# Kernel tuning notes

Hardware: AMD Instinct MI355X
Metric: run time of the kernel (lower is better)

## Reference

```python
import jax, jax.numpy as jnp
import numpy as np
from math import sqrt

D_MODEL = 1024
B, T = 4, 4096


def setup_inputs() -> dict:
    key = jax.random.key(0)
    kx, kqk, kvo = jax.random.split(key, 3)
    x = jax.random.normal(kx, (B, T, D_MODEL), dtype=jnp.float32)
    # xavier_uniform for square [D, D]: limit = sqrt(6 / (D + D))
    limit = sqrt(6.0 / (2 * D_MODEL))
    QK = jax.random.uniform(kqk, (D_MODEL, D_MODEL), minval=-limit, maxval=limit, dtype=jnp.float32)
    VO = jax.random.uniform(kvo, (D_MODEL, D_MODEL), minval=-limit, maxval=limit, dtype=jnp.float32)
    return {"x": x, "QK": QK, "VO": VO}


def reference(x, QK, VO):
    d_model = QK.shape[0]
    # scores[b,t,u] = x[b,t,:] @ QK @ x[b,u,:]  -- precompute xQK once
    xQK = jnp.einsum('btd,de->bte', x, QK)                 # [B,T,D]
    scores = jnp.einsum('bte,bue->btu', xQK, x) / sqrt(d_model)  # [B,T,T]
    attn = jax.nn.softmax(scores, axis=2)
    # out[b,t,e] = attn @ x @ VO
    av = jnp.einsum('btu,bud->btd', attn, x)               # [B,T,D]
    return jnp.einsum('btd,de->bte', av, VO)
```

## Files before the change

### kernel.cpp

```cpp
#include <hip/hip_runtime.h>
#include <hip/hip_bf16.h>


#define BB 4
#define TT 4096
#define DD 1024

typedef __attribute__((ext_vector_type(8))) short bf16x8;
typedef __attribute__((ext_vector_type(4))) float f32x4;

__device__ __forceinline__ void gll16(const void* g, void* l) {
  __builtin_amdgcn_global_load_lds(
      (__attribute__((address_space(1))) void*)g,
      (__attribute__((address_space(3))) void*)l, 16, 0, 0);
}

#define WAIT_VM(n) asm volatile("s_waitcnt vmcnt(" #n ")" ::: "memory")
#define WAIT_LGKM0 do { asm volatile("s_waitcnt lgkmcnt(0)" ::: "memory"); \
                        __builtin_amdgcn_sched_barrier(0); } while (0)
#define BARRIER    __builtin_amdgcn_s_barrier()

__global__ __launch_bounds__(256) void xprep_k(const float* __restrict__ in,
                                               __hip_bfloat16* __restrict__ rm,
                                               __hip_bfloat16* __restrict__ cm,
                                               int R, int C, long bs) {
  in += (long)blockIdx.z * bs; rm += (long)blockIdx.z * bs; cm += (long)blockIdx.z * bs;
  __shared__ __hip_bfloat16 tile[64][65];
  int c0 = blockIdx.x * 64, r0 = blockIdx.y * 64;
  int tx = threadIdx.x & 63, ty = threadIdx.x >> 6;
#pragma unroll
  for (int i = 0; i < 16; ++i) {
    int r = ty + i * 4;
    __hip_bfloat16 v = __float2bfloat16(in[(long)(r0 + r) * C + c0 + tx]);
    tile[r][tx] = v;
    rm[(long)(r0 + r) * C + c0 + tx] = v;
  }
  __syncthreads();
#pragma unroll
  for (int i = 0; i < 16; ++i) {
    int c = ty + i * 4;
    cm[(long)(c0 + c) * R + r0 + tx] = tile[tx][c];
  }
}

__global__ __launch_bounds__(256) void transpose_cast_k(const float* __restrict__ in,
                                                        __hip_bfloat16* __restrict__ out,
                                                        int R, int C) {
  __shared__ __hip_bfloat16 tile[64][65];
  int c0 = blockIdx.x * 64, r0 = blockIdx.y * 64;
  int tx = threadIdx.x & 63, ty = threadIdx.x >> 6;
#pragma unroll
  for (int i = 0; i < 16; ++i) {
    int r = ty + i * 4;
    tile[r][tx] = __float2bfloat16(in[(long)(r0 + r) * C + c0 + tx]);
  }
  __syncthreads();
#pragma unroll
  for (int i = 0; i < 16; ++i) {
    int c = ty + i * 4;
    out[(long)(c0 + c) * R + r0 + tx] = tile[tx][c];
  }
}

__global__ __launch_bounds__(256) void zero_f32_k(float* __restrict__ p, int n) {
  int i = blockIdx.x * 256 + threadIdx.x;
  if (i < n) p[i] = 0.f;
}

template <typename OUT_T, int EPI>
__global__ __launch_bounds__(512, 2) void gemm256(
    const __hip_bfloat16* __restrict__ A,
    const __hip_bfloat16* __restrict__ Bt,
    OUT_T* __restrict__ C,
    int M, int N, int K, float alpha,
    long sAz, long sBz, long sCz, float* __restrict__ lsum,
    int cx, int cy) {
  __shared__ alignas(16) char smem[131072];
  A  += (long)blockIdx.z * sAz;
  Bt += (long)blockIdx.z * sBz;
  C  += (long)blockIdx.z * sCz;

  const int lin = blockIdx.x + gridDim.x * blockIdx.y;
  const int xcd = lin & 7;
  const int s   = lin >> 3;
  const int rpc = cx * cy;
  const int r   = xcd + 8 * (s / rpc);
  const int p   = s % rpc;
  const int rx  = gridDim.x / cx;
  const int bx  = (r % rx) * cx + p % cx;
  const int by  = (r / rx) * cy + p / cx;

  const int tid  = threadIdx.x;
  const int lane = tid & 63;
  const int wid  = tid >> 6;
  const int wr   = wid >> 2;
  const int wc   = wid & 3;
  const long m0 = (long)bx * 256;
  const long n0 = (long)by * 256;
  const int NT = K >> 6;

  const int srow = tid >> 3;
  const int sswz = (tid & 7) ^ (srow & 7);
  const __hip_bfloat16* gA = A  + (m0 + srow) * (long)K + sswz * 8;
  const __hip_bfloat16* gB = Bt + (n0 + srow) * (long)K + sswz * 8;

#define STG_A(s_, c_, D_) gll16(gA + (long)(c_) * 64 * K + (long)(s_) * 64, \
                                smem + (D_) + (c_) * 8192 + wid * 1024)
#define STG_B(s_, c_, D_) gll16(gB + (long)(c_) * 64 * K + (long)(s_) * 64, \
                                smem + (D_) + 32768 + (c_) * 8192 + wid * 1024)

  const int fr = lane & 15, l4 = lane >> 4, f7 = lane & 7;
  const char* a00 = smem +         (wr * 128 + fr) * 128 + ((l4    ) ^ f7) * 16;
  const char* a01 = smem +         (wr * 128 + fr) * 128 + ((4 | l4) ^ f7) * 16;
  const char* b00 = smem + 32768 + (wc * 64  + fr) * 128 + ((l4    ) ^ f7) * 16;
  const char* b01 = smem + 32768 + (wc * 64  + fr) * 128 + ((4 | l4) ^ f7) * 16;
  const char* a10 = a00 + 65536; const char* a11 = a01 + 65536;
  const char* b10 = b00 + 65536; const char* b11 = b01 + 65536;

  bf16x8 aq[4][2], bq[4][2];
#define RD_A(p0, p1, MIOFF)                                         \
  _Pragma("unroll") for (int mi_ = 0; mi_ < 4; ++mi_) {             \
    aq[mi_][0] = *(const bf16x8*)((p0) + ((MIOFF) + mi_) * 2048);   \
    aq[mi_][1] = *(const bf16x8*)((p1) + ((MIOFF) + mi_) * 2048);   \
  }
#define RD_B(p0, p1, NI0)                                           \
  _Pragma("unroll") for (int ni_ = 0; ni_ < 2; ++ni_) {             \
    bq[(NI0) + ni_][0] = *(const bf16x8*)((p0) + ((NI0) + ni_) * 2048); \
    bq[(NI0) + ni_][1] = *(const bf16x8*)((p1) + ((NI0) + ni_) * 2048); \
  }

  f32x4 acc[8][4];
#pragma unroll
  for (int mi = 0; mi < 8; ++mi)
#pragma unroll
    for (int ni = 0; ni < 4; ++ni)
      acc[mi][ni] = (f32x4){0.f, 0.f, 0.f, 0.f};

#define MFMA16(MI0, NI0)                                                       \
  do {                                                                         \
    __builtin_amdgcn_s_setprio(1);                                             \
    _Pragma("unroll") for (int ks_ = 0; ks_ < 2; ++ks_)                        \
    _Pragma("unroll") for (int mi_ = 0; mi_ < 4; ++mi_)                        \
    _Pragma("unroll") for (int ni_ = 0; ni_ < 2; ++ni_)                        \
      acc[(MI0) + mi_][(NI0) + ni_] = __builtin_amdgcn_mfma_f32_16x16x32_bf16( \
          aq[mi_][ks_], bq[(NI0) + ni_][ks_], acc[(MI0) + mi_][(NI0) + ni_],   \
          0, 0, 0);                                                            \
    __builtin_amdgcn_s_setprio(0);                                             \
  } while (0)

#pragma unroll
  for (int c = 0; c < 4; ++c) STG_A(0, c, 0);
#pragma unroll
  for (int c = 0; c < 4; ++c) STG_B(0, c, 0);
  STG_B(1, 0, 65536); STG_B(1, 1, 65536);
  WAIT_VM(2);
  BARRIER;

  for (int t2 = 0; t2 < NT; t2 += 2) {
    const bool g = (t2 + 2 < NT);
    RD_A(a00, a01, 0); RD_B(b00, b01, 0);
    STG_B(t2 + 1, 2, 65536); STG_B(t2 + 1, 3, 65536);
    STG_A(t2 + 1, 0, 65536); STG_A(t2 + 1, 1, 65536);
    asm volatile("s_waitcnt lgkmcnt(8)");
    BARRIER; WAIT_LGKM0; MFMA16(0, 0);
    RD_B(b00, b01, 2);
    STG_A(t2 + 1, 2, 65536); STG_A(t2 + 1, 3, 65536);
    BARRIER; WAIT_LGKM0; MFMA16(0, 2);
    RD_A(a00, a01, 4);
    BARRIER; WAIT_LGKM0; MFMA16(4, 2);
    if (g) { STG_B(t2 + 2, 0, 0); STG_B(t2 + 2, 1, 0); WAIT_VM(2); }
    else   { WAIT_VM(0); }
    BARRIER; MFMA16(4, 0);
    RD_A(a10, a11, 0); RD_B(b10, b11, 0);
    if (g) { STG_B(t2 + 2, 2, 0); STG_B(t2 + 2, 3, 0);
             STG_A(t2 + 2, 0, 0); STG_A(t2 + 2, 1, 0); }
    asm volatile("s_waitcnt lgkmcnt(8)");
    BARRIER; WAIT_LGKM0; MFMA16(0, 0);
    RD_B(b10, b11, 2);
    if (g) { STG_A(t2 + 2, 2, 0); STG_A(t2 + 2, 3, 0); }
    BARRIER; WAIT_LGKM0; MFMA16(0, 2);
    RD_A(a10, a11, 4);
    BARRIER; WAIT_LGKM0; MFMA16(4, 2);
    if (g) { STG_B(t2 + 3, 0, 65536); STG_B(t2 + 3, 1, 65536); WAIT_VM(2); }
    BARRIER; MFMA16(4, 0);
  }

  if constexpr (EPI == 2) {
    float* lred = (float*)smem;
    __syncthreads();
    for (int i = tid; i < 1024; i += 512) lred[i] = 0.f;
    __syncthreads();
#pragma unroll
    for (int mi = 0; mi < 8; ++mi) {
#pragma unroll
      for (int r_ = 0; r_ < 4; ++r_) {
        const int rloc = wr * 128 + mi * 16 + (l4 << 2) + r_;
        const long row = m0 + rloc;
        float rs = 0.f;
#pragma unroll
        for (int ni = 0; ni < 4; ++ni) {
          float e = __expf(acc[mi][ni][r_] * alpha);
          long col = n0 + wc * 64 + ni * 16 + fr;
          C[row * (long)N + col] = (OUT_T)__float2bfloat16(e);
          rs += e;
        }
        rs += __shfl_xor(rs, 1); rs += __shfl_xor(rs, 2);
        rs += __shfl_xor(rs, 4); rs += __shfl_xor(rs, 8);
        if (fr == 0) lred[rloc * 4 + wc] = rs;
      }
    }
    __syncthreads();
    if (tid < 256) {
      float s4 = lred[tid * 4] + lred[tid * 4 + 1] + lred[tid * 4 + 2] + lred[tid * 4 + 3];
      atomicAdd(&lsum[(long)blockIdx.z * M + m0 + tid], s4);
    }
  } else if constexpr (EPI == 3) {
#pragma unroll
    for (int mi = 0; mi < 8; ++mi) {
      const long row = m0 + wr * 128 + mi * 16 + (l4 << 2);
      float4 lv = *(const float4*)&lsum[(long)blockIdx.z * M + row];
      float inv[4] = {1.f / lv.x, 1.f / lv.y, 1.f / lv.z, 1.f / lv.w};
#pragma unroll
      for (int ni = 0; ni < 4; ++ni) {
        long col = n0 + wc * 64 + ni * 16 + fr;
#pragma unroll
        for (int r_ = 0; r_ < 4; ++r_)
          C[(row + r_) * (long)N + col] = (OUT_T)__float2bfloat16(acc[mi][ni][r_] * inv[r_]);
      }
    }
  } else {
#pragma unroll
    for (int mi = 0; mi < 8; ++mi)
#pragma unroll
      for (int ni = 0; ni < 4; ++ni)
#pragma unroll
        for (int r_ = 0; r_ < 4; ++r_) {
          long row = m0 + wr * 128 + mi * 16 + (l4 << 2) + r_;
          long col = n0 + wc * 64 + ni * 16 + fr;
          float v = acc[mi][ni][r_] * alpha;
          if constexpr (EPI == 0)
            C[row * (long)N + col] = v;
          else
            C[row * (long)N + col] = (OUT_T)__float2bfloat16(v);
        }
  }
#undef STG_A
#undef STG_B
#undef RD_A
#undef RD_B
#undef MFMA16
}

extern "C" void kernel_launch(void* const* d_in, const int* in_sizes, int n_in,
                              void* d_out, int out_size, void* d_ws, size_t ws_size,
                              hipStream_t stream) {
  const float* x  = (const float*)d_in[0];
  const float* QK = (const float*)d_in[1];
  const float* VO = (const float*)d_in[2];
  char* ws = (char*)d_ws;

  const long MB = 1l << 20;
  __hip_bfloat16* QKT  = (__hip_bfloat16*)(ws);
  float*          lsum = (float*)(ws);
  __hip_bfloat16* VOT  = (__hip_bfloat16*)(ws + 2 * MB);
  __hip_bfloat16* xb   = (__hip_bfloat16*)(ws + 4 * MB);
  __hip_bfloat16* xT   = (__hip_bfloat16*)(ws + 36 * MB);
  __hip_bfloat16* attn = (__hip_bfloat16*)(ws + 68 * MB);
  __hip_bfloat16* xqk  = (__hip_bfloat16*)d_out;

  const long NTOK = (long)BB * TT;
  const long bstride = (long)TT * DD;
  const long aslot = (long)TT * TT;

  xprep_k<<<dim3(DD / 64, TT / 64, BB), 256, 0, stream>>>(x, xb, xT, TT, DD, bstride);
  transpose_cast_k<<<dim3(16, 16, 1), 256, 0, stream>>>(QK, QKT, DD, DD);
  transpose_cast_k<<<dim3(16, 16, 1), 256, 0, stream>>>(VO, VOT, DD, DD);

  gemm256<__hip_bfloat16, 1><<<dim3(TT / 256, DD / 256, BB), 512, 0, stream>>>(
      xb, QKT, xqk, TT, DD, DD, 1.0f, bstride, 0, bstride, nullptr, 2, 4);

  zero_f32_k<<<(int)(NTOK / 256), 256, 0, stream>>>(lsum, (int)NTOK);

  gemm256<__hip_bfloat16, 2><<<dim3(TT / 256, TT / 256, BB), 512, 0, stream>>>(
      xqk, xb, attn, TT, TT, DD, 0.03125f, bstride, bstride, aslot, lsum, 4, 8);

  gemm256<__hip_bfloat16, 3><<<dim3(TT / 256, DD / 256, BB), 512, 0, stream>>>(
      attn, xT, xb, TT, DD, TT, 1.0f, aslot, bstride, bstride, lsum, 2, 4);

  gemm256<float, 0><<<dim3((int)(NTOK / 256), DD / 256, 1), 512, 0, stream>>>(
      xb, VOT, (float*)d_out, (int)NTOK, DD, DD, 1.0f, 0, 0, 0, nullptr, 8, 4);
}
```

Before: 336.1 us.

## Software-pipeline LDS fragment reads ahead of MFMA blocks with double-buffered registers

Restructures the GEMM main loop so LDS reads for the next MFMA sub-block are issued before the current MFMA sub-block runs. A full 8-row A fragment set and two ping-pong B fragment buffers replace the single-use register arrays. Global-to-LDS staging of the next tile is reordered and waits are retuned, with A of tile 1 now prefetched in the prologue. The goal is to hide LDS latency behind matrix math, at the cost of more VGPRs and a trickier ordering of barriers and waits.

```diff
diff --git a/kernel.cpp b/kernel.cpp
--- a/kernel.cpp
+++ b/kernel.cpp
@@ -19,6 +19,7 @@
 #define WAIT_LGKM0 do { asm volatile("s_waitcnt lgkmcnt(0)" ::: "memory"); \
                         __builtin_amdgcn_sched_barrier(0); } while (0)
 #define BARRIER    __builtin_amdgcn_s_barrier()
+#define SB0        __builtin_amdgcn_sched_barrier(0)
 
 __global__ __launch_bounds__(256) void xprep_k(const float* __restrict__ in,
                                                __hip_bfloat16* __restrict__ rm,
@@ -117,16 +118,19 @@
   const char* a10 = a00 + 65536; const char* a11 = a01 + 65536;
   const char* b10 = b00 + 65536; const char* b11 = b01 + 65536;
 
-  bf16x8 aq[4][2], bq[4][2];
-#define RD_A(p0, p1, MIOFF)                                         \
-  _Pragma("unroll") for (int mi_ = 0; mi_ < 4; ++mi_) {             \
-    aq[mi_][0] = *(const bf16x8*)((p0) + ((MIOFF) + mi_) * 2048);   \
-    aq[mi_][1] = *(const bf16x8*)((p1) + ((MIOFF) + mi_) * 2048);   \
-  }
-#define RD_B(p0, p1, NI0)                                           \
-  _Pragma("unroll") for (int ni_ = 0; ni_ < 2; ++ni_) {             \
-    bq[(NI0) + ni_][0] = *(const bf16x8*)((p0) + ((NI0) + ni_) * 2048); \
-    bq[(NI0) + ni_][1] = *(const bf16x8*)((p1) + ((NI0) + ni_) * 2048); \
+  bf16x8 aq[8][2];
+  bf16x8 bqA[2][2];
+  bf16x8 bqB[2][2];
+
+#define RD_A4(p0, p1, MI0)                                                 \
+  _Pragma("unroll") for (int mi_ = 0; mi_ < 4; ++mi_) {                    \
+    aq[(MI0) + mi_][0] = *(const bf16x8*)((p0) + ((MI0) + mi_) * 2048);    \
+    aq[(MI0) + mi_][1] = *(const bf16x8*)((p1) + ((MI0) + mi_) * 2048);    \
+  }
+#define RD_B2(p0, p1, BQ, NB)                                              \
+  _Pragma("unroll") for (int ni_ = 0; ni_ < 2; ++ni_) {                    \
+    BQ[ni_][0] = *(const bf16x8*)((p0) + ((NB) + ni_) * 2048);             \
+    BQ[ni_][1] = *(const bf16x8*)((p1) + ((NB) + ni_) * 2048);             \
   }
 
   f32x4 acc[8][4];
@@ -136,14 +140,14 @@
     for (int ni = 0; ni < 4; ++ni)
       acc[mi][ni] = (f32x4){0.f, 0.f, 0.f, 0.f};
 
-#define MFMA16(MI0, NI0)                                                       \
+#define MFMA16(MI0, NI0, BQ)                                                   \
   do {                                                                         \
     __builtin_amdgcn_s_setprio(1);                                             \
     _Pragma("unroll") for (int ks_ = 0; ks_ < 2; ++ks_)                        \
     _Pragma("unroll") for (int mi_ = 0; mi_ < 4; ++mi_)                        \
     _Pragma("unroll") for (int ni_ = 0; ni_ < 2; ++ni_)                        \
       acc[(MI0) + mi_][(NI0) + ni_] = __builtin_amdgcn_mfma_f32_16x16x32_bf16( \
-          aq[mi_][ks_], bq[(NI0) + ni_][ks_], acc[(MI0) + mi_][(NI0) + ni_],   \
+          aq[(MI0) + mi_][ks_], BQ[ni_][ks_], acc[(MI0) + mi_][(NI0) + ni_],   \
           0, 0, 0);                                                            \
     __builtin_amdgcn_s_setprio(0);                                             \
   } while (0)
@@ -152,37 +156,60 @@
   for (int c = 0; c < 4; ++c) STG_A(0, c, 0);
 #pragma unroll
   for (int c = 0; c < 4; ++c) STG_B(0, c, 0);
+  STG_A(1, 0, 65536); STG_A(1, 1, 65536);
+  STG_A(1, 2, 65536); STG_A(1, 3, 65536);
   STG_B(1, 0, 65536); STG_B(1, 1, 65536);
-  WAIT_VM(2);
+  WAIT_VM(6);
   BARRIER;
+  RD_A4(a00, a01, 0);
+  RD_B2(b00, b01, bqA, 0);
 
   for (int t2 = 0; t2 < NT; t2 += 2) {
     const bool g = (t2 + 2 < NT);
-    RD_A(a00, a01, 0); RD_B(b00, b01, 0);
+    BARRIER; WAIT_LGKM0;
+    RD_A4(a00, a01, 4);
     STG_B(t2 + 1, 2, 65536); STG_B(t2 + 1, 3, 65536);
-    STG_A(t2 + 1, 0, 65536); STG_A(t2 + 1, 1, 65536);
-    asm volatile("s_waitcnt lgkmcnt(8)");
-    BARRIER; WAIT_LGKM0; MFMA16(0, 0);
-    RD_B(b00, b01, 2);
-    STG_A(t2 + 1, 2, 65536); STG_A(t2 + 1, 3, 65536);
-    BARRIER; WAIT_LGKM0; MFMA16(0, 2);
-    RD_A(a00, a01, 4);
-    BARRIER; WAIT_LGKM0; MFMA16(4, 2);
-    if (g) { STG_B(t2 + 2, 0, 0); STG_B(t2 + 2, 1, 0); WAIT_VM(2); }
-    else   { WAIT_VM(0); }
-    BARRIER; MFMA16(4, 0);
-    RD_A(a10, a11, 0); RD_B(b10, b11, 0);
-    if (g) { STG_B(t2 + 2, 2, 0); STG_B(t2 + 2, 3, 0);
-             STG_A(t2 + 2, 0, 0); STG_A(t2 + 2, 1, 0); }
-    asm volatile("s_waitcnt lgkmcnt(8)");
-    BARRIER; WAIT_LGKM0; MFMA16(0, 0);
-    RD_B(b10, b11, 2);
+    SB0;
+    MFMA16(0, 0, bqA);
+    BARRIER; WAIT_LGKM0;
+    RD_B2(b00, b01, bqB, 2);
+    if (g) { STG_A(t2 + 2, 0, 0); STG_A(t2 + 2, 1, 0); }
+    SB0;
+    MFMA16(4, 0, bqA);
+    BARRIER; WAIT_LGKM0;
     if (g) { STG_A(t2 + 2, 2, 0); STG_A(t2 + 2, 3, 0); }
-    BARRIER; WAIT_LGKM0; MFMA16(0, 2);
-    RD_A(a10, a11, 4);
-    BARRIER; WAIT_LGKM0; MFMA16(4, 2);
-    if (g) { STG_B(t2 + 3, 0, 65536); STG_B(t2 + 3, 1, 65536); WAIT_VM(2); }
-    BARRIER; MFMA16(4, 0);
+    SB0;
+    MFMA16(4, 2, bqB);
+    if (g) { WAIT_VM(4); } else { WAIT_VM(0); }
+    BARRIER; WAIT_LGKM0;
+    RD_A4(a10, a11, 4);
+    RD_B2(b10, b11, bqA, 0);
+    if (g) { STG_B(t2 + 2, 0, 0); STG_B(t2 + 2, 1, 0); }
+    SB0;
+    MFMA16(0, 2, bqB);
+    BARRIER; WAIT_LGKM0;
+    RD_A4(a10, a11, 0);
+    if (g) { STG_B(t2 + 2, 2, 0); STG_B(t2 + 2, 3, 0); }
+    SB0;
+    MFMA16(4, 0, bqA);
+    BARRIER; WAIT_LGKM0;
+    RD_B2(b10, b11, bqB, 2);
+    if (g) { STG_A(t2 + 3, 0, 65536); STG_A(t2 + 3, 1, 65536); }
+    SB0;
+    MFMA16(0, 0, bqA);
+    BARRIER; WAIT_LGKM0;
+    if (g) { STG_A(t2 + 3, 2, 65536); STG_A(t2 + 3, 3, 65536); }
+    SB0;
+    MFMA16(0, 2, bqB);
+    if (g) { WAIT_VM(4); }
+    BARRIER; WAIT_LGKM0;
+    if (g) {
+      RD_A4(a00, a01, 0);
+      RD_B2(b00, b01, bqA, 0);
+      STG_B(t2 + 3, 0, 65536); STG_B(t2 + 3, 1, 65536);
+    }
+    SB0;
+    MFMA16(4, 2, bqB);
   }
 
   if constexpr (EPI == 2) {
@@ -246,8 +273,8 @@
   }
 #undef STG_A
 #undef STG_B
-#undef RD_A
-#undef RD_B
+#undef RD_A4
+#undef RD_B2
 #undef MFMA16
 }
 
```

Measured after the change: 732.8 us. +118.0%, slower.
